# Performance work log

Hardware: AMD Instinct MI355X
Metric: run time of the kernel (lower is better)

## Reference

```python
import jax, jax.numpy as jnp
import numpy as np

N = 50000      # nodes
E = 800000     # edges
IN = 128       # in_channels
HID = 128      # hidden_channels
R = 8          # num_relations
B = 4          # num_bases
EPS = 1e-5     # BatchNorm eps


def setup_inputs() -> dict:
    key = jax.random.key(0)
    ks = jax.random.split(key, 16)
    s = 0.05
    f = jnp.float32
    return {
        "x": jax.random.normal(ks[0], (N, IN), f),
        "edge_index": jax.random.randint(ks[1], (2, E), 0, N),
        "edge_type": jax.random.randint(ks[2], (E,), 0, R),
        # conv1 (RGCNConv with basis decomposition): W_r = sum_b comp[r,b] * bases[b]
        "comp1": jax.random.normal(ks[3], (R, B), f) * s,
        "bases1": jax.random.normal(ks[4], (B, IN, HID), f) * s,
        "root1": jax.random.normal(ks[5], (IN, HID), f) * s,
        "bias1": jnp.zeros((HID,), f),
        # skip1: Linear(in, hidden)
        "skip1_w": jax.random.normal(ks[6], (IN, HID), f) * s,
        "skip1_b": jnp.zeros((HID,), f),
        # BatchNorm(hidden)
        "bn_gamma": jnp.ones((HID,), f),
        "bn_beta": jnp.zeros((HID,), f),
        # conv2
        "comp2": jax.random.normal(ks[7], (R, B), f) * s,
        "bases2": jax.random.normal(ks[8], (B, HID, HID), f) * s,
        "root2": jax.random.normal(ks[9], (HID, HID), f) * s,
        "bias2": jnp.zeros((HID,), f),
        # skip2: Linear(hidden, hidden)
        "skip2_w": jax.random.normal(ks[10], (HID, HID), f) * s,
        "skip2_b": jnp.zeros((HID,), f),
    }


def rgcn_conv(x, src, dst, etype, comp, bases, root, bias):
    """PyG RGCNConv: per-relation mean aggregation + root weight + bias."""
    # Basis decomposition: W [R, d_in, d_out]
    W = jnp.einsum('rb,bdf->rdf', comp, bases)
    # Transform all nodes under every relation (node-level GEMM, avoids [E,B,F])
    h = jnp.einsum('nd,rdf->rnf', x, W)          # [R, N, F]
    msg = h[etype, src]                           # [E, F] gather per edge
    # mean per (dst, relation): normalize by relation-specific in-degree
    seg = dst * R + etype                         # combined segment id
    cnt = jax.ops.segment_sum(jnp.ones((msg.shape[0],), x.dtype), seg,
                              num_segments=N * R)
    msg = msg * (1.0 / jnp.maximum(cnt, 1.0))[seg][:, None]
    agg = jax.ops.segment_sum(msg, dst, num_segments=N)  # sum over relations
    return agg + x @ root + bias


def reference(x, edge_index, edge_type,
              comp1, bases1, root1, bias1, skip1_w, skip1_b,
              bn_gamma, bn_beta,
              comp2, bases2, root2, bias2, skip2_w, skip2_b):
    src, dst = edge_index[0], edge_index[1]
    # layer 1: conv + skip
    x1 = rgcn_conv(x, src, dst, edge_type, comp1, bases1, root1, bias1) \
         + x @ skip1_w + skip1_b
    h = x1  # captured pre-BatchNorm (i == num_layers - 1 branch)
    # BatchNorm (training-style batch stats) + ReLU; dropout = identity (eval)
    m = x1.mean(axis=0)
    v = x1.var(axis=0)
    xn = bn_gamma * (x1 - m) / jnp.sqrt(v + EPS) + bn_beta
    xr = jax.nn.relu(xn)
    # final layer: conv + skip
    x2 = rgcn_conv(xr, src, dst, edge_type, comp2, bases2, root2, bias2) \
         + xr @ skip2_w + skip2_b
    return (h, x2)
```

## Files before the change

### kernel.cpp

```cpp
#include <hip/hip_runtime.h>
#include <hip/hip_bf16.h>

#define Nn   50000
#define Ee   800000
#define RR   8
#define CAP  64
#define EPSV 1e-5f
#define NBLK 782

typedef unsigned int   u32;
typedef unsigned short u16;
typedef __attribute__((ext_vector_type(8))) short bf16x8;
typedef __attribute__((ext_vector_type(4))) float f32x4;

typedef __attribute__((address_space(1))) const void gvoid;
typedef __attribute__((address_space(3))) void lvoid;

__device__ __forceinline__ void gl_lds16(const void* g, void* l) {
    __builtin_amdgcn_global_load_lds((gvoid*)g, (lvoid*)l, 16, 0, 0);
}

__device__ __forceinline__ float bf2f(u16 u) {
    return __uint_as_float(((u32)u) << 16);
}
__device__ __forceinline__ u16 f2bf(float f) {
    u32 x = __float_as_uint(f);
    u32 r = (x + 0x7FFFu + ((x >> 16) & 1u)) >> 16;
    return (u16)r;
}
__device__ __forceinline__ u32 pack2(float a, float b) {
    return (u32)f2bf(a) | ((u32)f2bf(b) << 16);
}

__global__ void __launch_bounds__(256) count_fill(const int* __restrict__ ei,
                                                  const int* __restrict__ et,
                                                  int* __restrict__ deg,
                                                  int* __restrict__ buckets) {
    int e = blockIdx.x * 256 + threadIdx.x;
    if (e >= Ee) return;
    int src = ei[e];
    int dst = ei[Ee + e];
    int rt  = et[e];
    int idx = atomicAdd(&deg[dst], 1);
    if (idx < CAP)
        __builtin_nontemporal_store((src & 0xFFFF) | (rt << 16),
                                    &buckets[dst * CAP + idx]);
}

__global__ void __launch_bounds__(256) cvt_bf16(const float2* __restrict__ xf,
                                                u32* __restrict__ xb) {
    int t = blockIdx.x * 256 + threadIdx.x;
    float2 v = xf[t];
    xb[t] = pack2(v.x, v.y);
}

__global__ void __launch_bounds__(256) prep_w(const float* __restrict__ bases,
                                              const float* __restrict__ root,
                                              const float* __restrict__ skipw,
                                              u16* __restrict__ wt) {
    int t = blockIdx.x * 256 + threadIdx.x;
    if (t >= 128 * 640) return;
    int c = t / 640, k = t % 640;
    float v;
    if (k < 512) {
        int b = k >> 7, kk = k & 127;
        v = bases[(b * 128 + kk) * 128 + c];
    } else {
        int kk = k - 512;
        v = root[kk * 128 + c] + skipw[kk * 128 + c];
    }
    wt[c * 640 + k] = f2bf(v);
}

__global__ void __launch_bounds__(256, 8) aggregate(const u32* __restrict__ xrow,
                                                    const float* __restrict__ comp,
                                                    const int* __restrict__ deg,
                                                    const int* __restrict__ buckets,
                                                    u32* __restrict__ xcat) {
    __shared__ int   bk_s[4][CAP];
    __shared__ float scale_s[4][32];
    int wv = threadIdx.x >> 6, lane = threadIdx.x & 63;
    int node = blockIdx.x * 4 + wv;

    int d = deg[node];
    d = d < CAP ? d : CAP;
    const int* bk = buckets + node * CAP;

    int w0 = 0;
    if (lane < d) { w0 = bk[lane]; bk_s[wv][lane] = w0; }

    int rt0 = (lane < d) ? (w0 >> 16) : 8;
    int c[RR];
#pragma unroll
    for (int r = 0; r < RR; r++) c[r] = __popcll(__ballot(rt0 == r));

    if (lane < 32) {
        int cc = c[lane >> 2];
        scale_s[wv][lane] = comp[lane] / (float)(cc < 1 ? 1 : cc);
    }
    __syncthreads();

    float a0 = 0, a1 = 0, b0 = 0, b1 = 0, c0 = 0, c1 = 0, d0 = 0, d1 = 0;
    int i = 0;
    for (; i + 4 <= d; i += 4) {
        int e0 = bk_s[wv][i], e1 = bk_s[wv][i + 1];
        int e2 = bk_s[wv][i + 2], e3 = bk_s[wv][i + 3];
        u32 x0 = xrow[(e0 & 0xFFFF) * 64 + lane];
        u32 x1 = xrow[(e1 & 0xFFFF) * 64 + lane];
        u32 x2 = xrow[(e2 & 0xFFFF) * 64 + lane];
        u32 x3 = xrow[(e3 & 0xFFFF) * 64 + lane];
        f32x4 s0 = *(const f32x4*)&scale_s[wv][(e0 >> 16) * 4];
        f32x4 s1 = *(const f32x4*)&scale_s[wv][(e1 >> 16) * 4];
        f32x4 s2 = *(const f32x4*)&scale_s[wv][(e2 >> 16) * 4];
        f32x4 s3 = *(const f32x4*)&scale_s[wv][(e3 >> 16) * 4];
        float v0, v1;
        v0 = bf2f((u16)x0); v1 = bf2f((u16)(x0 >> 16));
        a0 += s0[0] * v0; a1 += s0[0] * v1; b0 += s0[1] * v0; b1 += s0[1] * v1;
        c0 += s0[2] * v0; c1 += s0[2] * v1; d0 += s0[3] * v0; d1 += s0[3] * v1;
        v0 = bf2f((u16)x1); v1 = bf2f((u16)(x1 >> 16));
        a0 += s1[0] * v0; a1 += s1[0] * v1; b0 += s1[1] * v0; b1 += s1[1] * v1;
        c0 += s1[2] * v0; c1 += s1[2] * v1; d0 += s1[3] * v0; d1 += s1[3] * v1;
        v0 = bf2f((u16)x2); v1 = bf2f((u16)(x2 >> 16));
        a0 += s2[0] * v0; a1 += s2[0] * v1; b0 += s2[1] * v0; b1 += s2[1] * v1;
        c0 += s2[2] * v0; c1 += s2[2] * v1; d0 += s2[3] * v0; d1 += s2[3] * v1;
        v0 = bf2f((u16)x3); v1 = bf2f((u16)(x3 >> 16));
        a0 += s3[0] * v0; a1 += s3[0] * v1; b0 += s3[1] * v0; b1 += s3[1] * v1;
        c0 += s3[2] * v0; c1 += s3[2] * v1; d0 += s3[3] * v0; d1 += s3[3] * v1;
    }
    for (; i < d; i++) {
        int ee = bk_s[wv][i];
        u32 xv = xrow[(ee & 0xFFFF) * 64 + lane];
        f32x4 ss = *(const f32x4*)&scale_s[wv][(ee >> 16) * 4];
        float v0 = bf2f((u16)xv), v1 = bf2f((u16)(xv >> 16));
        a0 += ss[0] * v0; a1 += ss[0] * v1; b0 += ss[1] * v0; b1 += ss[1] * v1;
        c0 += ss[2] * v0; c1 += ss[2] * v1; d0 += ss[3] * v0; d1 += ss[3] * v1;
    }

    u32* orow = xcat + node * 320;
    orow[0 * 64 + lane] = pack2(a0, a1);
    orow[1 * 64 + lane] = pack2(b0, b1);
    orow[2 * 64 + lane] = pack2(c0, c1);
    orow[3 * 64 + lane] = pack2(d0, d1);
    orow[256 + lane]    = xrow[node * 64 + lane];
}

__global__ void __launch_bounds__(256) gemm_x(const u16* __restrict__ xcat,
                                              const u16* __restrict__ wt,
                                              const float* __restrict__ biasA,
                                              const float* __restrict__ biasB,
                                              float* __restrict__ out,
                                              float* __restrict__ bnsum,
                                              int do_stats) {
    __shared__ u16 As[64 * 64];
    __shared__ u16 Bs[128 * 64];

    int t = threadIdx.x, w = t >> 6, lane = t & 63;
    int m0 = blockIdx.x * 64;
    int lm = lane & 15, hk = lane >> 4;

    const u16* agp[2]; char* alp[2];
#pragma unroll
    for (int j = 0; j < 2; j++) {
        int f = j * 256 + t;
        int row = f >> 3, kc = (f & 7) ^ (row & 7);
        int gr = m0 + row; gr = gr < Nn ? gr : Nn - 1;
        agp[j] = xcat + gr * 640 + kc * 8;
        alp[j] = (char*)As + j * 4096 + w * 1024;
    }
    const u16* bgp[4]; char* blp[4];
#pragma unroll
    for (int j = 0; j < 4; j++) {
        int f = j * 256 + t;
        int col = f >> 3, kc = (f & 7) ^ (col & 7);
        bgp[j] = wt + col * 640 + kc * 8;
        blp[j] = (char*)Bs + j * 4096 + w * 1024;
    }

    int wr = (w & 1) * 32, wc = (w >> 1) * 64;
    f32x4 acc[2][4];
#pragma unroll
    for (int f = 0; f < 2; f++)
#pragma unroll
        for (int g = 0; g < 4; g++) acc[f][g] = (f32x4){0, 0, 0, 0};

    for (int it = 0; it < 10; it++) {
        int ko = it * 64;
#pragma unroll
        for (int j = 0; j < 2; j++) gl_lds16(agp[j] + ko, alp[j]);
#pragma unroll
        for (int j = 0; j < 4; j++) gl_lds16(bgp[j] + ko, blp[j]);
        __syncthreads();
#pragma unroll
        for (int ks = 0; ks < 2; ks++) {
            int sw = (((ks * 4 + hk) ^ (lm & 7)) * 16);
            bf16x8 a0 = *(const bf16x8*)((const char*)As + (wr + lm) * 128 + sw);
            bf16x8 a1 = *(const bf16x8*)((const char*)As + (wr + 16 + lm) * 128 + sw);
            bf16x8 b0 = *(const bf16x8*)((const char*)Bs + (wc + lm) * 128 + sw);
            bf16x8 b1 = *(const bf16x8*)((const char*)Bs + (wc + 16 + lm) * 128 + sw);
            bf16x8 b2 = *(const bf16x8*)((const char*)Bs + (wc + 32 + lm) * 128 + sw);
            bf16x8 b3 = *(const bf16x8*)((const char*)Bs + (wc + 48 + lm) * 128 + sw);
            acc[0][0] = __builtin_amdgcn_mfma_f32_16x16x32_bf16(a0, b0, acc[0][0], 0, 0, 0);
            acc[1][0] = __builtin_amdgcn_mfma_f32_16x16x32_bf16(a1, b0, acc[1][0], 0, 0, 0);
            acc[0][1] = __builtin_amdgcn_mfma_f32_16x16x32_bf16(a0, b1, acc[0][1], 0, 0, 0);
            acc[1][1] = __builtin_amdgcn_mfma_f32_16x16x32_bf16(a1, b1, acc[1][1], 0, 0, 0);
            acc[0][2] = __builtin_amdgcn_mfma_f32_16x16x32_bf16(a0, b2, acc[0][2], 0, 0, 0);
            acc[1][2] = __builtin_amdgcn_mfma_f32_16x16x32_bf16(a1, b2, acc[1][2], 0, 0, 0);
            acc[0][3] = __builtin_amdgcn_mfma_f32_16x16x32_bf16(a0, b3, acc[0][3], 0, 0, 0);
            acc[1][3] = __builtin_amdgcn_mfma_f32_16x16x32_bf16(a1, b3, acc[1][3], 0, 0, 0);
        }
        __syncthreads();
    }

    float bias[4];
#pragma unroll
    for (int g = 0; g < 4; g++) {
        int cc = wc + g * 16 + lm;
        bias[g] = biasA[cc] + biasB[cc];
    }
    float lsum[4] = {0, 0, 0, 0}, lsq[4] = {0, 0, 0, 0};
#pragma unroll
    for (int fr = 0; fr < 2; fr++)
#pragma unroll
        for (int g = 0; g < 4; g++)
#pragma unroll
            for (int i = 0; i < 4; i++) {
                int grow = m0 + wr + fr * 16 + hk * 4 + i;
                if (grow < Nn) {
                    float v = acc[fr][g][i] + bias[g];
                    out[grow * 128 + wc + g * 16 + lm] = v;
                    lsum[g] += v; lsq[g] += v * v;
                }
            }
    if (do_stats) {
#pragma unroll
        for (int g = 0; g < 4; g++) {
            lsum[g] += __shfl_xor(lsum[g], 16); lsum[g] += __shfl_xor(lsum[g], 32);
            lsq[g]  += __shfl_xor(lsq[g], 16);  lsq[g]  += __shfl_xor(lsq[g], 32);
        }
        if (hk == 0) {
#pragma unroll
            for (int g = 0; g < 4; g++) {
                int cc = wc + g * 16 + lm;
                atomicAdd(&bnsum[cc], lsum[g]);
                atomicAdd(&bnsum[128 + cc], lsq[g]);
            }
        }
    }
}

__global__ void bn_final(const float* __restrict__ bnsum,
                         const float* __restrict__ gamma,
                         const float* __restrict__ beta,
                         float* __restrict__ ab) {
    int c = threadIdx.x;
    float m   = bnsum[c] * (1.0f / Nn);
    float ex2 = bnsum[128 + c] * (1.0f / Nn);
    float var = ex2 - m * m;
    float s   = gamma[c] / sqrtf(var + EPSV);
    ab[c]       = s;
    ab[128 + c] = beta[c] - m * s;
}

__global__ void __launch_bounds__(256) bn_relu(const float2* __restrict__ h,
                                               const float* __restrict__ ab,
                                               u32* __restrict__ xr) {
    int t = blockIdx.x * 256 + threadIdx.x;
    int c0 = (t & 63) * 2;
    float2 hv = h[t];
    float v0 = hv.x * ab[c0] + ab[128 + c0];
    float v1 = hv.y * ab[c0 + 1] + ab[128 + c0 + 1];
    v0 = v0 > 0.f ? v0 : 0.f;
    v1 = v1 > 0.f ? v1 : 0.f;
    xr[t] = pack2(v0, v1);
}

extern "C" void kernel_launch(void* const* d_in, const int* in_sizes, int n_in,
                              void* d_out, int out_size, void* d_ws, size_t ws_size,
                              hipStream_t stream) {
    const float* x      = (const float*)d_in[0];
    const int*   ei     = (const int*)d_in[1];
    const int*   et     = (const int*)d_in[2];
    const float* comp1  = (const float*)d_in[3];
    const float* bases1 = (const float*)d_in[4];
    const float* root1  = (const float*)d_in[5];
    const float* bias1  = (const float*)d_in[6];
    const float* skip1w = (const float*)d_in[7];
    const float* skip1b = (const float*)d_in[8];
    const float* gamma  = (const float*)d_in[9];
    const float* beta   = (const float*)d_in[10];
    const float* comp2  = (const float*)d_in[11];
    const float* bases2 = (const float*)d_in[12];
    const float* root2  = (const float*)d_in[13];
    const float* bias2  = (const float*)d_in[14];
    const float* skip2w = (const float*)d_in[15];
    const float* skip2b = (const float*)d_in[16];
    float* out = (float*)d_out;

    char* ws = (char*)d_ws;
    int*   deg     = (int*)(ws + 0);
    float* bnsum   = (float*)(ws + 200000);
    float* ab      = (float*)(ws + 201024);
    int*   buckets = (int*)(ws + 202240);
    u16*   wt1     = (u16*)(ws + 13002240);
    u16*   wt2     = (u16*)(ws + 13166080);
    u32*   xb      = (u32*)(ws + 13329920);
    u32*   xr      = xb;
    u16*   xcat    = (u16*)(ws + 26129920);

    hipMemsetAsync(deg, 0, 201024, stream);

    count_fill<<<(Ee + 255) / 256, 256, 0, stream>>>(ei, et, deg, buckets);
    prep_w<<<320, 256, 0, stream>>>(bases1, root1, skip1w, wt1);
    prep_w<<<320, 256, 0, stream>>>(bases2, root2, skip2w, wt2);
    cvt_bf16<<<Nn / 4, 256, 0, stream>>>((const float2*)x, xb);

    aggregate<<<Nn / 4, 256, 0, stream>>>(xb, comp1, deg, buckets, (u32*)xcat);
    gemm_x<<<NBLK, 256, 0, stream>>>(xcat, wt1, bias1, skip1b, out, bnsum, 1);

    bn_final<<<1, 128, 0, stream>>>(bnsum, gamma, beta, ab);
    bn_relu<<<Nn / 4, 256, 0, stream>>>((const float2*)out, ab, xr);

    aggregate<<<Nn / 4, 256, 0, stream>>>(xr, comp2, deg, buckets, (u32*)xcat);
    gemm_x<<<NBLK, 256, 0, stream>>>(xcat, wt2, bias2, skip2b, out + Nn * 128, bnsum, 0);
}
```

Measured before the change: 331.9 us.

## Double-buffer GEMM tiles, drop xcat self-copy, use readlane in aggregation

The aggregate kernel stops copying each node's own features into the concatenated buffer. The GEMM now reads the last K chunks straight from the bf16 feature array, which removes a write and re-read of 128 columns per node. The GEMM tile loop is double-buffered in 48KB of LDS, so the loads for the next K step are issued before the MFMAs of the current one, cutting one barrier per iteration. Aggregation replaces the LDS staging of bucket entries and scales with wave readlane broadcasts and unrolls by 8 to keep more gathers in flight. The larger LDS footprint may reduce GEMM occupancy.

```diff
diff --git a/kernel.cpp b/kernel.cpp
--- a/kernel.cpp
+++ b/kernel.cpp
@@ -30,6 +30,9 @@
 }
 __device__ __forceinline__ u32 pack2(float a, float b) {
     return (u32)f2bf(a) | ((u32)f2bf(b) << 16);
+}
+__device__ __forceinline__ float rdlane_f(float v, int idx) {
+    return __uint_as_float(__builtin_amdgcn_readlane(__float_as_uint(v), idx));
 }
 
 __global__ void __launch_bounds__(256) count_fill(const int* __restrict__ ei,
@@ -76,104 +79,96 @@
                                                     const float* __restrict__ comp,
                                                     const int* __restrict__ deg,
                                                     const int* __restrict__ buckets,
-                                                    u32* __restrict__ xcat) {
-    __shared__ int   bk_s[4][CAP];
-    __shared__ float scale_s[4][32];
+                                                    u32* __restrict__ xcat5) {
     int wv = threadIdx.x >> 6, lane = threadIdx.x & 63;
     int node = blockIdx.x * 4 + wv;
 
     int d = deg[node];
     d = d < CAP ? d : CAP;
-    const int* bk = buckets + node * CAP;
-
-    int w0 = 0;
-    if (lane < d) { w0 = bk[lane]; bk_s[wv][lane] = w0; }
+    int w0 = (lane < d) ? buckets[node * CAP + lane] : 0;
 
     int rt0 = (lane < d) ? (w0 >> 16) : 8;
     int c[RR];
 #pragma unroll
     for (int r = 0; r < RR; r++) c[r] = __popcll(__ballot(rt0 == r));
-
+    float sc = 0.0f;
     if (lane < 32) {
         int cc = c[lane >> 2];
-        scale_s[wv][lane] = comp[lane] / (float)(cc < 1 ? 1 : cc);
-    }
-    __syncthreads();
+        sc = comp[lane] / (float)(cc < 1 ? 1 : cc);
+    }
 
     float a0 = 0, a1 = 0, b0 = 0, b1 = 0, c0 = 0, c1 = 0, d0 = 0, d1 = 0;
     int i = 0;
-    for (; i + 4 <= d; i += 4) {
-        int e0 = bk_s[wv][i], e1 = bk_s[wv][i + 1];
-        int e2 = bk_s[wv][i + 2], e3 = bk_s[wv][i + 3];
-        u32 x0 = xrow[(e0 & 0xFFFF) * 64 + lane];
-        u32 x1 = xrow[(e1 & 0xFFFF) * 64 + lane];
-        u32 x2 = xrow[(e2 & 0xFFFF) * 64 + lane];
-        u32 x3 = xrow[(e3 & 0xFFFF) * 64 + lane];
-        f32x4 s0 = *(const f32x4*)&scale_s[wv][(e0 >> 16) * 4];
-        f32x4 s1 = *(const f32x4*)&scale_s[wv][(e1 >> 16) * 4];
-        f32x4 s2 = *(const f32x4*)&scale_s[wv][(e2 >> 16) * 4];
-        f32x4 s3 = *(const f32x4*)&scale_s[wv][(e3 >> 16) * 4];
-        float v0, v1;
-        v0 = bf2f((u16)x0); v1 = bf2f((u16)(x0 >> 16));
-        a0 += s0[0] * v0; a1 += s0[0] * v1; b0 += s0[1] * v0; b1 += s0[1] * v1;
-        c0 += s0[2] * v0; c1 += s0[2] * v1; d0 += s0[3] * v0; d1 += s0[3] * v1;
-        v0 = bf2f((u16)x1); v1 = bf2f((u16)(x1 >> 16));
-        a0 += s1[0] * v0; a1 += s1[0] * v1; b0 += s1[1] * v0; b1 += s1[1] * v1;
-        c0 += s1[2] * v0; c1 += s1[2] * v1; d0 += s1[3] * v0; d1 += s1[3] * v1;
-        v0 = bf2f((u16)x2); v1 = bf2f((u16)(x2 >> 16));
-        a0 += s2[0] * v0; a1 += s2[0] * v1; b0 += s2[1] * v0; b1 += s2[1] * v1;
-        c0 += s2[2] * v0; c1 += s2[2] * v1; d0 += s2[3] * v0; d1 += s2[3] * v1;
-        v0 = bf2f((u16)x3); v1 = bf2f((u16)(x3 >> 16));
-        a0 += s3[0] * v0; a1 += s3[0] * v1; b0 += s3[1] * v0; b1 += s3[1] * v1;
-        c0 += s3[2] * v0; c1 += s3[2] * v1; d0 += s3[3] * v0; d1 += s3[3] * v1;
+    for (; i + 8 <= d; i += 8) {
+        u32 g[8]; int rt[8];
+#pragma unroll
+        for (int j = 0; j < 8; j++) {
+            int e = __builtin_amdgcn_readlane(w0, i + j);
+            rt[j] = (e >> 16) & 7;
+            g[j]  = xrow[(e & 0xFFFF) * 64 + lane];
+        }
+#pragma unroll
+        for (int j = 0; j < 8; j++) {
+            float s0 = rdlane_f(sc, rt[j] * 4 + 0);
+            float s1 = rdlane_f(sc, rt[j] * 4 + 1);
+            float s2 = rdlane_f(sc, rt[j] * 4 + 2);
+            float s3 = rdlane_f(sc, rt[j] * 4 + 3);
+            float v0 = bf2f((u16)g[j]), v1 = bf2f((u16)(g[j] >> 16));
+            a0 += s0 * v0; a1 += s0 * v1; b0 += s1 * v0; b1 += s1 * v1;
+            c0 += s2 * v0; c1 += s2 * v1; d0 += s3 * v0; d1 += s3 * v1;
+        }
     }
     for (; i < d; i++) {
-        int ee = bk_s[wv][i];
-        u32 xv = xrow[(ee & 0xFFFF) * 64 + lane];
-        f32x4 ss = *(const f32x4*)&scale_s[wv][(ee >> 16) * 4];
-        float v0 = bf2f((u16)xv), v1 = bf2f((u16)(xv >> 16));
-        a0 += ss[0] * v0; a1 += ss[0] * v1; b0 += ss[1] * v0; b1 += ss[1] * v1;
-        c0 += ss[2] * v0; c1 += ss[2] * v1; d0 += ss[3] * v0; d1 += ss[3] * v1;
-    }
-
-    u32* orow = xcat + node * 320;
+        int e  = __builtin_amdgcn_readlane(w0, i);
+        int rt = (e >> 16) & 7;
+        u32 g  = xrow[(e & 0xFFFF) * 64 + lane];
+        float s0 = rdlane_f(sc, rt * 4 + 0);
+        float s1 = rdlane_f(sc, rt * 4 + 1);
+        float s2 = rdlane_f(sc, rt * 4 + 2);
+        float s3 = rdlane_f(sc, rt * 4 + 3);
+        float v0 = bf2f((u16)g), v1 = bf2f((u16)(g >> 16));
+        a0 += s0 * v0; a1 += s0 * v1; b0 += s1 * v0; b1 += s1 * v1;
+        c0 += s2 * v0; c1 += s2 * v1; d0 += s3 * v0; d1 += s3 * v1;
+    }
+
+    u32* orow = xcat5 + node * 256;
     orow[0 * 64 + lane] = pack2(a0, a1);
     orow[1 * 64 + lane] = pack2(b0, b1);
     orow[2 * 64 + lane] = pack2(c0, c1);
     orow[3 * 64 + lane] = pack2(d0, d1);
-    orow[256 + lane]    = xrow[node * 64 + lane];
-}
-
-__global__ void __launch_bounds__(256) gemm_x(const u16* __restrict__ xcat,
+}
+
+__global__ void __launch_bounds__(256) gemm_x(const u16* __restrict__ xcat5,
+                                              const u16* __restrict__ xb16,
                                               const u16* __restrict__ wt,
                                               const float* __restrict__ biasA,
                                               const float* __restrict__ biasB,
                                               float* __restrict__ out,
                                               float* __restrict__ bnsum,
                                               int do_stats) {
-    __shared__ u16 As[64 * 64];
-    __shared__ u16 Bs[128 * 64];
+    __shared__ char sm[49152];
 
     int t = threadIdx.x, w = t >> 6, lane = t & 63;
     int m0 = blockIdx.x * 64;
     int lm = lane & 15, hk = lane >> 4;
 
-    const u16* agp[2]; char* alp[2];
+    const u16* agpx[2]; const u16* agpb[2]; int alo[2];
 #pragma unroll
     for (int j = 0; j < 2; j++) {
         int f = j * 256 + t;
         int row = f >> 3, kc = (f & 7) ^ (row & 7);
         int gr = m0 + row; gr = gr < Nn ? gr : Nn - 1;
-        agp[j] = xcat + gr * 640 + kc * 8;
-        alp[j] = (char*)As + j * 4096 + w * 1024;
-    }
-    const u16* bgp[4]; char* blp[4];
+        agpx[j] = xcat5 + gr * 512 + kc * 8;
+        agpb[j] = xb16 + gr * 128 + kc * 8;
+        alo[j]  = j * 4096 + w * 1024;
+    }
+    const u16* bgp[4]; int blo[4];
 #pragma unroll
     for (int j = 0; j < 4; j++) {
         int f = j * 256 + t;
         int col = f >> 3, kc = (f & 7) ^ (col & 7);
         bgp[j] = wt + col * 640 + kc * 8;
-        blp[j] = (char*)Bs + j * 4096 + w * 1024;
+        blo[j] = 8192 + j * 4096 + w * 1024;
     }
 
     int wr = (w & 1) * 32, wc = (w >> 1) * 64;
@@ -183,22 +178,39 @@
 #pragma unroll
         for (int g = 0; g < 4; g++) acc[f][g] = (f32x4){0, 0, 0, 0};
 
+    {
+#pragma unroll
+        for (int j = 0; j < 2; j++) gl_lds16(agpx[j], sm + alo[j]);
+#pragma unroll
+        for (int j = 0; j < 4; j++) gl_lds16(bgp[j], sm + blo[j]);
+    }
+    __syncthreads();
+
     for (int it = 0; it < 10; it++) {
-        int ko = it * 64;
-#pragma unroll
-        for (int j = 0; j < 2; j++) gl_lds16(agp[j] + ko, alp[j]);
-#pragma unroll
-        for (int j = 0; j < 4; j++) gl_lds16(bgp[j] + ko, blp[j]);
-        __syncthreads();
+        if (it < 9) {
+            int nit = it + 1;
+            char* nb = sm + (nit & 1) * 24576;
+            if (nit < 8) {
+#pragma unroll
+                for (int j = 0; j < 2; j++) gl_lds16(agpx[j] + nit * 64, nb + alo[j]);
+            } else {
+#pragma unroll
+                for (int j = 0; j < 2; j++) gl_lds16(agpb[j] + (nit - 8) * 64, nb + alo[j]);
+            }
+#pragma unroll
+            for (int j = 0; j < 4; j++) gl_lds16(bgp[j] + nit * 64, nb + blo[j]);
+        }
+        const char* Ab = sm + (it & 1) * 24576;
+        const char* Bb = Ab + 8192;
 #pragma unroll
         for (int ks = 0; ks < 2; ks++) {
             int sw = (((ks * 4 + hk) ^ (lm & 7)) * 16);
-            bf16x8 a0 = *(const bf16x8*)((const char*)As + (wr + lm) * 128 + sw);
-            bf16x8 a1 = *(const bf16x8*)((const char*)As + (wr + 16 + lm) * 128 + sw);
-            bf16x8 b0 = *(const bf16x8*)((const char*)Bs + (wc + lm) * 128 + sw);
-            bf16x8 b1 = *(const bf16x8*)((const char*)Bs + (wc + 16 + lm) * 128 + sw);
-            bf16x8 b2 = *(const bf16x8*)((const char*)Bs + (wc + 32 + lm) * 128 + sw);
-            bf16x8 b3 = *(const bf16x8*)((const char*)Bs + (wc + 48 + lm) * 128 + sw);
+            bf16x8 a0 = *(const bf16x8*)(Ab + (wr + lm) * 128 + sw);
+            bf16x8 a1 = *(const bf16x8*)(Ab + (wr + 16 + lm) * 128 + sw);
+            bf16x8 b0 = *(const bf16x8*)(Bb + (wc + lm) * 128 + sw);
+            bf16x8 b1 = *(const bf16x8*)(Bb + (wc + 16 + lm) * 128 + sw);
+            bf16x8 b2 = *(const bf16x8*)(Bb + (wc + 32 + lm) * 128 + sw);
+            bf16x8 b3 = *(const bf16x8*)(Bb + (wc + 48 + lm) * 128 + sw);
             acc[0][0] = __builtin_amdgcn_mfma_f32_16x16x32_bf16(a0, b0, acc[0][0], 0, 0, 0);
             acc[1][0] = __builtin_amdgcn_mfma_f32_16x16x32_bf16(a1, b0, acc[1][0], 0, 0, 0);
             acc[0][1] = __builtin_amdgcn_mfma_f32_16x16x32_bf16(a0, b1, acc[0][1], 0, 0, 0);
@@ -208,7 +220,7 @@
             acc[0][3] = __builtin_amdgcn_mfma_f32_16x16x32_bf16(a0, b3, acc[0][3], 0, 0, 0);
             acc[1][3] = __builtin_amdgcn_mfma_f32_16x16x32_bf16(a1, b3, acc[1][3], 0, 0, 0);
         }
-        __syncthreads();
+        if (it < 9) __syncthreads();
     }
 
     float bias[4];
@@ -305,7 +317,7 @@
     u16*   wt2     = (u16*)(ws + 13166080);
     u32*   xb      = (u32*)(ws + 13329920);
     u32*   xr      = xb;
-    u16*   xcat    = (u16*)(ws + 26129920);
+    u16*   xcat5   = (u16*)(ws + 26129920);
 
     hipMemsetAsync(deg, 0, 201024, stream);
 
@@ -314,12 +326,14 @@
     prep_w<<<320, 256, 0, stream>>>(bases2, root2, skip2w, wt2);
     cvt_bf16<<<Nn / 4, 256, 0, stream>>>((const float2*)x, xb);
 
-    aggregate<<<Nn / 4, 256, 0, stream>>>(xb, comp1, deg, buckets, (u32*)xcat);
-    gemm_x<<<NBLK, 256, 0, stream>>>(xcat, wt1, bias1, skip1b, out, bnsum, 1);
+    aggregate<<<Nn / 4, 256, 0, stream>>>(xb, comp1, deg, buckets, (u32*)xcat5);
+    gemm_x<<<NBLK, 256, 0, stream>>>(xcat5, (const u16*)xb, wt1, bias1, skip1b,
+                                     out, bnsum, 1);
 
     bn_final<<<1, 128, 0, stream>>>(bnsum, gamma, beta, ab);
     bn_relu<<<Nn / 4, 256, 0, stream>>>((const float2*)out, ab, xr);
 
-    aggregate<<<Nn / 4, 256, 0, stream>>>(xr, comp2, deg, buckets, (u32*)xcat);
-    gemm_x<<<NBLK, 256, 0, stream>>>(xcat, wt2, bias2, skip2b, out + Nn * 128, bnsum, 0);
-}
+    aggregate<<<Nn / 4, 256, 0, stream>>>(xr, comp2, deg, buckets, (u32*)xcat5);
+    gemm_x<<<NBLK, 256, 0, stream>>>(xcat5, (const u16*)xr, wt2, bias2, skip2b,
+                                     out + Nn * 128, bnsum, 0);
+}
```

New measurement: 338.2 us. Within noise of the previous version (+1.9%).
